# Performance work log

Hardware: AMD Instinct MI355X
Metric: run time of the kernel (lower is better)

The kernel has to match this reference:

```python
import jax, jax.numpy as jnp
import numpy as np

B, S, E, H = 4, 2048, 1024, 16
D = E // H  # head dim = 64
STRIDE, EXPR = 128, 32


def build_sparse_mask(S, stride=STRIDE, expr=EXPR):
    """Fairseq SparseMultiheadAttention fixed pattern, is_bidirectional=False.
    True = attention allowed (mask value 0), False = -inf."""
    def ckpt(i):
        if i % stride == 0 and i != 0:
            return i - expr
        return (i // stride) * stride + stride - expr

    def summaries(amax):
        s = set()
        c = ckpt(0)
        while c <= amax - 1:
            s.update(range(c, min(c + expr + 1, amax)))
            c = ckpt(c + stride)
        return s

    m = np.zeros((S, S), dtype=bool)
    for i in range(S):
        amax = i + 1  # causal (not bidirectional)
        r = ((i + stride) // stride) * stride
        if i % stride == 0 and i != 0:
            one = set(range(i - stride, min(amax, i + 1)))
        else:
            one = set(range(max(0, r - stride), min(amax, r + 1)))
        idx = sorted(one | summaries(amax))
        m[i, idx] = True
    return m


def setup_inputs() -> dict:
    key = jax.random.key(0)
    ks = jax.random.split(key, 12)
    sc = 0.02
    inp = {
        "x": jax.random.normal(ks[0], (B, S, E), dtype=jnp.float32),
        "ln1_g": jnp.ones((E,), jnp.float32), "ln1_b": jnp.zeros((E,), jnp.float32),
        "ln2_g": jnp.ones((E,), jnp.float32), "ln2_b": jnp.zeros((E,), jnp.float32),
        "wq": jax.random.normal(ks[1], (E, E), jnp.float32) * sc, "bq": jnp.zeros((E,), jnp.float32),
        "wk": jax.random.normal(ks[2], (E, E), jnp.float32) * sc, "bk": jnp.zeros((E,), jnp.float32),
        "wv": jax.random.normal(ks[3], (E, E), jnp.float32) * sc, "bv": jnp.zeros((E,), jnp.float32),
        "wo": jax.random.normal(ks[4], (E, E), jnp.float32) * sc, "bo": jnp.zeros((E,), jnp.float32),
        "w_fc": jax.random.normal(ks[5], (4 * E, E), jnp.float32) * sc, "b_fc": jnp.zeros((4 * E,), jnp.float32),
        "w_proj": jax.random.normal(ks[6], (E, 4 * E), jnp.float32) * sc, "b_proj": jnp.zeros((E,), jnp.float32),
        "mask": jnp.asarray(build_sparse_mask(S)),
    }
    return inp


def _ln(x, g, b, eps=1e-5):
    mu = jnp.mean(x, axis=-1, keepdims=True)
    var = jnp.var(x, axis=-1, keepdims=True)
    return (x - mu) * jax.lax.rsqrt(var + eps) * g + b


def _new_gelu(x):
    c = np.sqrt(2.0 / np.pi).astype(np.float32)
    return 0.5 * x * (1.0 + jnp.tanh(c * (x + 0.044715 * x ** 3)))


def reference(x, ln1_g, ln1_b, ln2_g, ln2_b, wq, bq, wk, bk, wv, bv, wo, bo,
              w_fc, b_fc, w_proj, b_proj, mask):
    # x: [B,S,E]. Note: Block residual uses ln_1(x), not raw x (x is reassigned).
    h = _ln(x, ln1_g, ln1_b)
    scale = D ** -0.5
    q = ((h @ wq.T + bq) * scale).reshape(B, S, H, D)
    k = (h @ wk.T + bk).reshape(B, S, H, D)
    v = (h @ wv.T + bv).reshape(B, S, H, D)
    scores = jnp.einsum("bqhd,bkhd->bhqk", q, k)
    scores = jnp.where(mask[None, None], scores, -jnp.inf)  # fixed sparse pattern
    p = jax.nn.softmax(scores, axis=-1)
    attn = jnp.einsum("bhqk,bkhd->bqhd", p, v).reshape(B, S, E)
    attn = attn @ wo.T + bo
    h = h + attn
    # MLP (dropout in eval mode = identity)
    y = _new_gelu(_ln(h, ln2_g, ln2_b) @ w_fc.T + b_fc) @ w_proj.T + b_proj
    return h + y
```

## Files before the change

kernel.cpp:

```cpp
#include <hip/hip_runtime.h>
#include <hip/hip_bf16.h>

#define B_ 4
#define S_ 2048
#define E_ 1024
#define H_ 16
#define D_ 64

typedef __bf16 bf16x8 __attribute__((ext_vector_type(8)));
typedef __bf16 bf16x4 __attribute__((ext_vector_type(4)));
typedef float  f32x4  __attribute__((ext_vector_type(4)));

__device__ __forceinline__ void gl_lds16(const void* g, void* l) {
  __builtin_amdgcn_global_load_lds((const __attribute__((address_space(1))) void*)g,
                                   (__attribute__((address_space(3))) void*)l, 16, 0, 0);
}

__global__ __launch_bounds__(256) void ln_kernel(const float* __restrict__ x,
                                                 const float* __restrict__ g,
                                                 const float* __restrict__ b,
                                                 float* __restrict__ o,
                                                 __bf16* __restrict__ ohi,
                                                 __bf16* __restrict__ olo) {
  int row = blockIdx.x;
  int t = threadIdx.x;
  const float* xr = x + (size_t)row * E_;
  float4 v = *(const float4*)(xr + t * 4);
  float s  = v.x + v.y + v.z + v.w;
  float ss = v.x * v.x + v.y * v.y + v.z * v.z + v.w * v.w;
#pragma unroll
  for (int off = 1; off < 64; off <<= 1) {
    s  += __shfl_xor(s, off);
    ss += __shfl_xor(ss, off);
  }
  __shared__ float sh[8];
  if ((t & 63) == 0) { sh[t >> 6] = s; sh[4 + (t >> 6)] = ss; }
  __syncthreads();
  s  = sh[0] + sh[1] + sh[2] + sh[3];
  ss = sh[4] + sh[5] + sh[6] + sh[7];
  float mu  = s * (1.0f / E_);
  float var = ss * (1.0f / E_) - mu * mu;
  float rstd = rsqrtf(var + 1e-5f);
  float4 gg = *(const float4*)(g + t * 4);
  float4 bb = *(const float4*)(b + t * 4);
  float ov[4];
  ov[0] = (v.x - mu) * rstd * gg.x + bb.x;
  ov[1] = (v.y - mu) * rstd * gg.y + bb.y;
  ov[2] = (v.z - mu) * rstd * gg.z + bb.z;
  ov[3] = (v.w - mu) * rstd * gg.w + bb.w;
  size_t base = (size_t)row * E_ + t * 4;
  if (o) *(float4*)(o + base) = make_float4(ov[0], ov[1], ov[2], ov[3]);
  if (ohi) {
    bf16x4 hv, lv;
#pragma unroll
    for (int j = 0; j < 4; ++j) {
      __bf16 hh = (__bf16)ov[j];
      hv[j] = hh;
      lv[j] = (__bf16)(ov[j] - (float)hh);
    }
    *(bf16x4*)(ohi + base) = hv;
    *(bf16x4*)(olo + base) = lv;
  }
}

__global__ __launch_bounds__(256) void split_kernel(const float* __restrict__ in,
                                                    __bf16* __restrict__ hi,
                                                    __bf16* __restrict__ lo,
                                                    int n4) {
  int idx = blockIdx.x * 256 + threadIdx.x;
  int stride = gridDim.x * 256;
  for (int i = idx; i < n4; i += stride) {
    float4 v = ((const float4*)in)[i];
    bf16x4 hv, lv;
#pragma unroll
    for (int j = 0; j < 4; ++j) {
      float f = (&v.x)[j];
      __bf16 hh = (__bf16)f;
      hv[j] = hh;
      lv[j] = (__bf16)(f - (float)hh);
    }
    ((bf16x4*)hi)[i] = hv;
    ((bf16x4*)lo)[i] = lv;
  }
}

template <int BM>
__global__ __launch_bounds__(512, 2) void gemm3(
    const __bf16* __restrict__ Ah, const __bf16* __restrict__ Al,
    const __bf16* __restrict__ Bh, const __bf16* __restrict__ Bl,
    int N, int K,
    const float* __restrict__ b0, const float* __restrict__ b1,
    const float* __restrict__ b2,
    const float* __restrict__ res, float* __restrict__ Cf,
    __bf16* __restrict__ C0h, __bf16* __restrict__ C0l,
    __bf16* __restrict__ C1h, __bf16* __restrict__ C1l,
    __bf16* __restrict__ C2h, __bf16* __restrict__ C2l,
    int act, int qkv) {
  constexpr int MI    = BM / 32;
  constexpr int MPP   = MI / 4;
  constexpr int AR    = BM / 64;
  constexpr int RND   = AR + 4;
  constexpr int AU    = BM * 8;
  constexpr int BUFU  = AU + 2048;
  constexpr int MTLOG = (BM == 256) ? 5 : 6;
  constexpr int LOGBM = (BM == 256) ? 8 : 7;

  __shared__ bf16x8 lds[2 * BUFU];

  const int t = threadIdx.x;
  const int l = t & 63;
  const int w = t >> 6;
  const int wr = w >> 2, wc = w & 3;
  const int fr = l & 15, kq = l >> 4;

  const int nwg = gridDim.x;
  const int cpx = nwg >> 3;
  const int bid = blockIdx.x;
  const int swz = (bid & 7) * cpx + (bid >> 3);
  const int mt  = swz & ((1 << MTLOG) - 1);
  const int ntl = swz >> MTLOG;
  const int row0 = mt * BM, col0 = ntl * 256;

  const int ktp = K >> 6;
  const int nt3 = 3 * ktp;

  f32x4 acc[MI][4];
#pragma unroll
  for (int i = 0; i < MI; ++i)
#pragma unroll
    for (int j = 0; j < 4; ++j) acc[i][j] = (f32x4){0.f, 0.f, 0.f, 0.f};

  auto STAGE = [&](const __bf16* Ax, const __bf16* Bx, int k0, int q, int buf) {
    if (q < AR) {
      int u = q * 512 + t;
      int row = u & (BM - 1), kg = u >> LOGBM;
      gl_lds16(Ax + (size_t)(row0 + row) * K + k0 + kg * 8,
               &lds[buf * BUFU + q * 512 + (t & 448)]);
    } else {
      int qb = q - AR;
      int u = qb * 512 + t;
      int col = u & 255, kg = u >> 8;
      gl_lds16(Bx + (size_t)(col0 + col) * K + k0 + kg * 8,
               &lds[buf * BUFU + AU + qb * 512 + (t & 448)]);
    }
  };

#pragma unroll
  for (int q = 0; q < RND; ++q) STAGE(Ah, Bh, 0, q, 0);

  int cur = 0;
  int k0n = 64, pn = 0;
  if (ktp == 1) { k0n = 0; pn = 1; }

  for (int kt = 0; kt < nt3; ++kt) {
    const bool notlast = (kt + 1 < nt3);
    const __bf16* An = (pn == 2) ? Al : Ah;
    const __bf16* Bn = (pn == 1) ? Bl : Bh;
    const int nxt = cur ^ 1;
    bf16x8 bfr[4][2];
#pragma unroll
    for (int p = 0; p < 4; ++p) {
      if (notlast) {
        if (2 * p < RND)     STAGE(An, Bn, k0n, 2 * p, nxt);
        if (2 * p + 1 < RND) STAGE(An, Bn, k0n, 2 * p + 1, nxt);
      }
      if (p == 0) {
        if (notlast) asm volatile("s_waitcnt vmcnt(2)" ::: "memory");
        else         asm volatile("s_waitcnt vmcnt(0)" ::: "memory");
        __builtin_amdgcn_s_barrier();
        asm volatile("" ::: "memory");
#pragma unroll
        for (int ni = 0; ni < 4; ++ni)
#pragma unroll
          for (int ks = 0; ks < 2; ++ks)
            bfr[ni][ks] = lds[cur * BUFU + AU + (ks * 4 + kq) * 256 + wc * 64 + ni * 16 + fr];
      }
      bf16x8 af[MPP][2];
#pragma unroll
      for (int mm = 0; mm < MPP; ++mm)
#pragma unroll
        for (int ks = 0; ks < 2; ++ks)
          af[mm][ks] = lds[cur * BUFU + (ks * 4 + kq) * BM + wr * (BM / 2) + (p * MPP + mm) * 16 + fr];
      __builtin_amdgcn_s_setprio(1);
#pragma unroll
      for (int mm = 0; mm < MPP; ++mm)
#pragma unroll
        for (int ni = 0; ni < 4; ++ni)
#pragma unroll
          for (int ks = 0; ks < 2; ++ks)
            acc[p * MPP + mm][ni] = __builtin_amdgcn_mfma_f32_16x16x32_bf16(
                af[mm][ks], bfr[ni][ks], acc[p * MPP + mm][ni], 0, 0, 0);
      __builtin_amdgcn_s_setprio(0);
    }
    asm volatile("" ::: "memory");
    __builtin_amdgcn_s_barrier();
    asm volatile("" ::: "memory");
    cur = nxt;
    k0n += 64;
    if (k0n == K) { k0n = 0; ++pn; }
  }

#pragma unroll
  for (int mi = 0; mi < MI; ++mi) {
    const int rowb = row0 + wr * (BM / 2) + mi * 16 + kq * 4;
#pragma unroll
    for (int ni = 0; ni < 4; ++ni) {
      const int col = col0 + wc * 64 + ni * 16 + fr;
#pragma unroll
      for (int r = 0; r < 4; ++r) {
        const int grow = rowb + r;
        float v = acc[mi][ni][r];
        if (qkv) {
          const int seg = col >> 10, ci = col & 1023;
          float bias = (seg == 0) ? b0[ci] : (seg == 1) ? b1[ci] : b2[ci];
          v += bias;
          if (seg == 0) v *= 0.125f;
          __bf16 hh = (__bf16)v;
          __bf16 ll = (__bf16)(v - (float)hh);
          size_t off = (size_t)grow * 1024 + ci;
          if (seg == 0)      { C0h[off] = hh; C0l[off] = ll; }
          else if (seg == 1) { C1h[off] = hh; C1l[off] = ll; }
          else {
            int bb2 = grow >> 11, ii = grow & 2047;
            int h2i = ci >> 6, dd = ci & 63;
            size_t offt = ((((size_t)bb2 * H_ + h2i) * D_ + dd) << 11) + ii;
            C2h[offt] = hh; C2l[offt] = ll;
          }
        } else {
          v += b0[col];
          if (act) {
            float zn = 0.7978845608028654f * (v + 0.044715f * v * v * v);
            float e = __expf(fminf(2.f * zn, 80.f));
            v = v * e / (e + 1.f);
          }
          size_t off = (size_t)grow * N + col;
          if (res) v += res[off];
          if (Cf) Cf[off] = v;
          if (C0h) {
            __bf16 hh = (__bf16)v;
            C0h[off] = hh;
            C0l[off] = (__bf16)(v - (float)hh);
          }
        }
      }
    }
  }
}

__device__ __forceinline__ bool sp_allowed(int i, int j) {
  if (j > i) return false;
  bool local;
  if ((i & 127) == 0 && i != 0) local = (j >= i - 128);
  else                          local = (j >= ((i >> 7) << 7));
  int jm = j & 127;
  bool summ = (j >= 96) && ((jm >= 96) || (jm == 0 && j >= 128));
  return local || summ;
}

__global__ __launch_bounds__(256) void attn_mfma(
    const __bf16* __restrict__ qhi, const __bf16* __restrict__ qlo,
    const __bf16* __restrict__ khi, const __bf16* __restrict__ klo,
    const __bf16* __restrict__ vth, const __bf16* __restrict__ vtl,
    __bf16* __restrict__ abhi, __bf16* __restrict__ ablo) {
  const int qt = blockIdx.x;
  const int h  = blockIdx.y;
  const int b  = blockIdx.z;
  const int t = threadIdx.x;
  const int l = t & 63;
  const int w = t >> 6;
  const int lanelo = l & 15, lanehi = l >> 4;

  __shared__ bf16x8 KhL[512], KlL[512], VhL[512], VlL[512];
  __shared__ __align__(16) __bf16 Pl[4][16][72];

  const int arow = qt * 64 + w * 16 + lanelo;
  size_t qoff = ((size_t)(b * S_ + arow)) * E_ + h * D_ + lanehi * 8;
  bf16x8 qh[2], ql[2];
  qh[0] = *(const bf16x8*)(qhi + qoff);      qh[1] = *(const bf16x8*)(qhi + qoff + 32);
  ql[0] = *(const bf16x8*)(qlo + qoff);      ql[1] = *(const bf16x8*)(qlo + qoff + 32);

  const int drow = qt * 64 + w * 16 + lanehi * 4;

  f32x4 o_acc[4];
#pragma unroll
  for (int n = 0; n < 4; ++n) o_acc[n] = (f32x4){0.f, 0.f, 0.f, 0.f};
  float mrow[4] = {-1e30f, -1e30f, -1e30f, -1e30f};
  float lrow[4] = {0.f, 0.f, 0.f, 0.f};

  const int nnear0 = (qt >= 2) ? (qt - 2) : 0;
  const int L = (qt - 2) * 64;
  int tmax = 0, nfar = 0;
  if (L > 96) {
    tmax = (L - 96 + 127) >> 7;
    nfar = (5 * tmax + 7) >> 3;
  }
  const int ntiles = nfar + (qt - nnear0 + 1);

  for (int tile = 0; tile < ntiles; ++tile) {
    const bool is_far = tile < nfar;
    const int jb = nnear0 + (tile - nfar);

    if (w < 2) {
      int c = l, jg; bool valid;
      if (is_far) {
        unsigned g8 = tile * 8 + (c >> 3);
        unsigned t5 = g8 / 5u, u = g8 - t5 * 5u;
        int oo = (int)(u * 8) + (c & 7);
        jg = 96 + ((int)t5 << 7) + oo;
        valid = (g8 < 5u * (unsigned)tmax) && (oo <= 32) && (jg < L);
      } else { jg = (jb << 6) + c; valid = true; }
      int tok = b * S_ + (valid ? jg : 0);
      const __bf16* src = (w == 0 ? khi : klo) + (size_t)tok * E_ + h * D_;
      bf16x8* dst = (w == 0 ? KhL : KlL);
#pragma unroll
      for (int dg = 0; dg < 8; ++dg) gl_lds16(src + dg * 8, dst + dg * 64);
    } else {
      const __bf16* src = (w == 2 ? vth : vtl) + ((size_t)((b * H_ + h) * D_ + l)) * S_;
      bf16x8* dst = (w == 2 ? VhL : VlL);
#pragma unroll
      for (int jgp = 0; jgp < 8; ++jgp) {
        int j0;
        if (is_far) {
          unsigned g8 = tile * 8 + jgp;
          unsigned t5 = g8 / 5u, u = g8 - t5 * 5u;
          j0 = (g8 < 5u * (unsigned)tmax) ? (96 + ((int)t5 << 7) + (int)u * 8) : 0;
        } else j0 = (jb << 6) + jgp * 8;
        gl_lds16(src + j0, dst + jgp * 64);
      }
    }
    __syncthreads();

    f32x4 s[4];
#pragma unroll
    for (int n = 0; n < 4; ++n) s[n] = (f32x4){0.f, 0.f, 0.f, 0.f};
#pragma unroll
    for (int ks = 0; ks < 2; ++ks) {
#pragma unroll
      for (int n = 0; n < 4; ++n) {
        bf16x8 kb_h = KhL[(4 * ks + lanehi) * 64 + n * 16 + lanelo];
        bf16x8 kb_l = KlL[(4 * ks + lanehi) * 64 + n * 16 + lanelo];
        s[n] = __builtin_amdgcn_mfma_f32_16x16x32_bf16(qh[ks], kb_h, s[n], 0, 0, 0);
        s[n] = __builtin_amdgcn_mfma_f32_16x16x32_bf16(qh[ks], kb_l, s[n], 0, 0, 0);
        s[n] = __builtin_amdgcn_mfma_f32_16x16x32_bf16(ql[ks], kb_h, s[n], 0, 0, 0);
      }
    }

    int jgc[4]; bool vldc[4], summc[4];
#pragma unroll
    for (int n = 0; n < 4; ++n) {
      int c = n * 16 + lanelo;
      if (is_far) {
        unsigned g8 = tile * 8 + (c >> 3);
        unsigned t5 = g8 / 5u, u = g8 - t5 * 5u;
        int oo = (int)(u * 8) + (c & 7);
        int jg = 96 + ((int)t5 << 7) + oo;
        jgc[n] = jg;
        vldc[n] = (g8 < 5u * (unsigned)tmax) && (oo <= 32) && (jg < L);
        summc[n] = true;
      } else {
        int jg = (jb << 6) + c;
        jgc[n] = jg; vldc[n] = true;
        int jm = jg & 127;
        summc[n] = (jg >= 96) && ((jm >= 96) || (jm == 0 && jg >= 128));
      }
    }
    float tm[4] = {-1e30f, -1e30f, -1e30f, -1e30f};
#pragma unroll
    for (int r = 0; r < 4; ++r) {
      int i = drow + r;
      int lb = (((i & 127) == 0) && i != 0) ? (i - 128) : ((i >> 7) << 7);
#pragma unroll
      for (int n = 0; n < 4; ++n) {
        bool ok = is_far ? vldc[n]
                         : ((jgc[n] <= i) && ((jgc[n] >= lb) || summc[n]));
        float sv = ok ? s[n][r] : -1e30f;
        s[n][r] = sv;
        tm[r] = fmaxf(tm[r], sv);
      }
    }
#pragma unroll
    for (int off = 1; off < 16; off <<= 1)
#pragma unroll
      for (int r = 0; r < 4; ++r) tm[r] = fmaxf(tm[r], __shfl_xor(tm[r], off));

    float psum[4] = {0.f, 0.f, 0.f, 0.f};
#pragma unroll
    for (int r = 0; r < 4; ++r) {
      float mnew = fmaxf(mrow[r], tm[r]);
      float alpha = __expf(mrow[r] - mnew);
      mrow[r] = mnew;
      lrow[r] *= alpha;
#pragma unroll
      for (int n = 0; n < 4; ++n) o_acc[n][r] *= alpha;
#pragma unroll
      for (int n = 0; n < 4; ++n) {
        float sv = s[n][r];
        float p = (sv > -1e29f) ? __expf(sv - mnew) : 0.f;
        s[n][r] = p;
        psum[r] += p;
      }
    }
#pragma unroll
    for (int off = 1; off < 16; off <<= 1)
#pragma unroll
      for (int r = 0; r < 4; ++r) psum[r] += __shfl_xor(psum[r], off);
#pragma unroll
    for (int r = 0; r < 4; ++r) lrow[r] += psum[r];

#pragma unroll
    for (int r = 0; r < 4; ++r)
#pragma unroll
      for (int n = 0; n < 4; ++n)
        Pl[w][lanehi * 4 + r][n * 16 + lanelo] = (__bf16)s[n][r];
    bf16x8 pa[2];
    pa[0] = *(const bf16x8*)&Pl[w][lanelo][8 * lanehi];
    pa[1] = *(const bf16x8*)&Pl[w][lanelo][8 * lanehi + 32];

#pragma unroll
    for (int ks = 0; ks < 2; ++ks) {
#pragma unroll
      for (int n = 0; n < 4; ++n) {
        bf16x8 vb_h = VhL[(4 * ks + lanehi) * 64 + n * 16 + lanelo];
        bf16x8 vb_l = VlL[(4 * ks + lanehi) * 64 + n * 16 + lanelo];
        o_acc[n] = __builtin_amdgcn_mfma_f32_16x16x32_bf16(pa[ks], vb_h, o_acc[n], 0, 0, 0);
        o_acc[n] = __builtin_amdgcn_mfma_f32_16x16x32_bf16(pa[ks], vb_l, o_acc[n], 0, 0, 0);
      }
    }
    __syncthreads();
  }

#pragma unroll
  for (int r = 0; r < 4; ++r) {
    float inv = 1.0f / lrow[r];
    int i = drow + r;
    size_t rb = ((size_t)(b * S_ + i)) * E_ + h * D_;
#pragma unroll
    for (int n = 0; n < 4; ++n) {
      float val = o_acc[n][r] * inv;
      __bf16 hh = (__bf16)val;
      abhi[rb + n * 16 + lanelo] = hh;
      ablo[rb + n * 16 + lanelo] = (__bf16)(val - (float)hh);
    }
  }
}

extern "C" void kernel_launch(void* const* d_in, const int* in_sizes, int n_in,
                              void* d_out, int out_size, void* d_ws, size_t ws_size,
                              hipStream_t stream) {
  const float* x      = (const float*)d_in[0];
  const float* ln1_g  = (const float*)d_in[1];
  const float* ln1_b  = (const float*)d_in[2];
  const float* ln2_g  = (const float*)d_in[3];
  const float* ln2_b  = (const float*)d_in[4];
  const float* wq     = (const float*)d_in[5];
  const float* bq     = (const float*)d_in[6];
  const float* wk     = (const float*)d_in[7];
  const float* bk     = (const float*)d_in[8];
  const float* wv     = (const float*)d_in[9];
  const float* bv     = (const float*)d_in[10];
  const float* wo     = (const float*)d_in[11];
  const float* bo     = (const float*)d_in[12];
  const float* w_fc   = (const float*)d_in[13];
  const float* b_fc   = (const float*)d_in[14];
  const float* w_proj = (const float*)d_in[15];
  const float* b_proj = (const float*)d_in[16];

  char* W = (char*)d_ws;
  const size_t MB = (size_t)1 << 20;
  const int NTOK = B_ * S_;

  float*  h      = (float*)(W + 0 * MB);
  __bf16* h_hi   = (__bf16*)(W + 32 * MB);
  __bf16* h_lo   = (__bf16*)(W + 48 * MB);
  __bf16* q_hi   = (__bf16*)(W + 64 * MB);
  __bf16* q_lo   = (__bf16*)(W + 80 * MB);
  __bf16* k_hi   = (__bf16*)(W + 96 * MB);
  __bf16* k_lo   = (__bf16*)(W + 112 * MB);
  __bf16* vt_hi  = (__bf16*)(W + 128 * MB);
  __bf16* vt_lo  = (__bf16*)(W + 144 * MB);
  __bf16* ab_hi  = h_hi;
  __bf16* ab_lo  = h_lo;
  float*  h2     = (float*)(W + 64 * MB);
  __bf16* l2o_hi = (__bf16*)(W + 0 * MB);
  __bf16* l2o_lo = (__bf16*)(W + 16 * MB);
  __bf16* fcb_hi = (__bf16*)(W + 96 * MB);
  __bf16* fcb_lo = (__bf16*)(W + 160 * MB);
  __bf16* wqkv_hi = (__bf16*)(W + 160 * MB);
  __bf16* wqkv_lo = (__bf16*)(W + 166 * MB);
  __bf16* wo_hi  = (__bf16*)(W + 172 * MB);
  __bf16* wo_lo  = (__bf16*)(W + 174 * MB);
  __bf16* wfc_hi = (__bf16*)(W + 32 * MB);
  __bf16* wfc_lo = (__bf16*)(W + 40 * MB);
  __bf16* wpj_hi = (__bf16*)(W + 32 * MB);
  __bf16* wpj_lo = (__bf16*)(W + 40 * MB);
  float* out = (float*)d_out;

  const int SPLIT_BLKS = 2048;
  const int nw1 = E_ * E_ / 4;
  const int nw4 = 4 * E_ * E_ / 4;
  const int WSEG = E_ * E_;

  ln_kernel<<<NTOK, 256, 0, stream>>>(x, ln1_g, ln1_b, h, h_hi, h_lo);

  split_kernel<<<SPLIT_BLKS, 256, 0, stream>>>(wq, wqkv_hi, wqkv_lo, nw1);
  split_kernel<<<SPLIT_BLKS, 256, 0, stream>>>(wk, wqkv_hi + WSEG, wqkv_lo + WSEG, nw1);
  split_kernel<<<SPLIT_BLKS, 256, 0, stream>>>(wv, wqkv_hi + 2 * WSEG, wqkv_lo + 2 * WSEG, nw1);
  gemm3<256><<<384, 512, 0, stream>>>(h_hi, h_lo, wqkv_hi, wqkv_lo, 3072, E_,
                                      bq, bk, bv, nullptr, nullptr,
                                      q_hi, q_lo, k_hi, k_lo, vt_hi, vt_lo, 0, 1);

  attn_mfma<<<dim3(S_ / 64, H_, B_), 256, 0, stream>>>(q_hi, q_lo, k_hi, k_lo,
                                                       vt_hi, vt_lo, ab_hi, ab_lo);

  split_kernel<<<SPLIT_BLKS, 256, 0, stream>>>(wo, wo_hi, wo_lo, nw1);
  gemm3<128><<<256, 512, 0, stream>>>(ab_hi, ab_lo, wo_hi, wo_lo, E_, E_,
                                      bo, nullptr, nullptr, h, h2,
                                      nullptr, nullptr, nullptr, nullptr, nullptr, nullptr, 0, 0);

  ln_kernel<<<NTOK, 256, 0, stream>>>(h2, ln2_g, ln2_b, nullptr, l2o_hi, l2o_lo);

  split_kernel<<<SPLIT_BLKS, 256, 0, stream>>>(w_fc, wfc_hi, wfc_lo, nw4);
  gemm3<256><<<512, 512, 0, stream>>>(l2o_hi, l2o_lo, wfc_hi, wfc_lo, 4 * E_, E_,
                                      b_fc, nullptr, nullptr, nullptr, nullptr,
                                      fcb_hi, fcb_lo, nullptr, nullptr, nullptr, nullptr, 1, 0);

  split_kernel<<<SPLIT_BLKS, 256, 0, stream>>>(w_proj, wpj_hi, wpj_lo, nw4);
  gemm3<128><<<256, 512, 0, stream>>>(fcb_hi, fcb_lo, wpj_hi, wpj_lo, E_, 4 * E_,
                                      b_proj, nullptr, nullptr, h2, out,
                                      nullptr, nullptr, nullptr, nullptr, nullptr, nullptr, 0, 0);
}
```

Measured before the change: 1.469 ms.

## Restructure GEMM k-loop into four barrier-separated phases interleaving staging and MFMA

Splits each 64-wide k-tile in the hi/lo split-bf16 GEMM into four phases, one per k-half and m-half pair. Each phase loads its own A fragments and, where needed, B fragments from LDS. Global-to-LDS staging for the next tile is issued after each phase's LDS reads, and a barrier separates phases. The aim is to smooth memory/compute interleaving and reduce register pressure from double-held fragments, at the cost of more barriers per tile.

After: 1.496 ms. About the same (+1.8%).

```diff
diff --git a/kernel.cpp b/kernel.cpp
--- a/kernel.cpp
+++ b/kernel.cpp
@@ -85,7 +85,7 @@
 }
 
 template <int BM>
-__global__ __launch_bounds__(512, 2) void gemm3(
+__global__ __launch_bounds__(512, 2) void gemm8(
     const __bf16* __restrict__ Ah, const __bf16* __restrict__ Al,
     const __bf16* __restrict__ Bh, const __bf16* __restrict__ Bl,
     int N, int K,
@@ -97,7 +97,7 @@
     __bf16* __restrict__ C2h, __bf16* __restrict__ C2l,
     int act, int qkv) {
   constexpr int MI    = BM / 32;
-  constexpr int MPP   = MI / 4;
+  constexpr int MH    = MI / 2;
   constexpr int AR    = BM / 64;
   constexpr int RND   = AR + 4;
   constexpr int AU    = BM * 8;
@@ -157,44 +157,51 @@
     const __bf16* An = (pn == 2) ? Al : Ah;
     const __bf16* Bn = (pn == 1) ? Bl : Bh;
     const int nxt = cur ^ 1;
-    bf16x8 bfr[4][2];
+    bf16x8 bfr[4];
 #pragma unroll
     for (int p = 0; p < 4; ++p) {
-      if (notlast) {
-        if (2 * p < RND)     STAGE(An, Bn, k0n, 2 * p, nxt);
-        if (2 * p + 1 < RND) STAGE(An, Bn, k0n, 2 * p + 1, nxt);
-      }
+      const int ks = p >> 1, mh = p & 1;
+      bf16x8 af[MH];
       if (p == 0) {
-        if (notlast) asm volatile("s_waitcnt vmcnt(2)" ::: "memory");
-        else         asm volatile("s_waitcnt vmcnt(0)" ::: "memory");
+        if (notlast) {
+          STAGE(An, Bn, k0n, 0, nxt);
+          STAGE(An, Bn, k0n, 1, nxt);
+          asm volatile("s_waitcnt vmcnt(2)" ::: "memory");
+        } else {
+          asm volatile("s_waitcnt vmcnt(0)" ::: "memory");
+        }
         __builtin_amdgcn_s_barrier();
-        asm volatile("" ::: "memory");
 #pragma unroll
         for (int ni = 0; ni < 4; ++ni)
-#pragma unroll
-          for (int ks = 0; ks < 2; ++ks)
-            bfr[ni][ks] = lds[cur * BUFU + AU + (ks * 4 + kq) * 256 + wc * 64 + ni * 16 + fr];
-      }
-      bf16x8 af[MPP][2];
-#pragma unroll
-      for (int mm = 0; mm < MPP; ++mm)
-#pragma unroll
-        for (int ks = 0; ks < 2; ++ks)
-          af[mm][ks] = lds[cur * BUFU + (ks * 4 + kq) * BM + wr * (BM / 2) + (p * MPP + mm) * 16 + fr];
+          bfr[ni] = lds[cur * BUFU + AU + (ks * 4 + kq) * 256 + wc * 64 + ni * 16 + fr];
+#pragma unroll
+        for (int mm = 0; mm < MH; ++mm)
+          af[mm] = lds[cur * BUFU + (ks * 4 + kq) * BM + wr * (BM / 2) + (mh * MH + mm) * 16 + fr];
+      } else {
+        if (mh == 0) {
+#pragma unroll
+          for (int ni = 0; ni < 4; ++ni)
+            bfr[ni] = lds[cur * BUFU + AU + (ks * 4 + kq) * 256 + wc * 64 + ni * 16 + fr];
+        }
+#pragma unroll
+        for (int mm = 0; mm < MH; ++mm)
+          af[mm] = lds[cur * BUFU + (ks * 4 + kq) * BM + wr * (BM / 2) + (mh * MH + mm) * 16 + fr];
+        if (notlast) {
+          if (2 * p < RND)     STAGE(An, Bn, k0n, 2 * p, nxt);
+          if (2 * p + 1 < RND) STAGE(An, Bn, k0n, 2 * p + 1, nxt);
+        }
+        __builtin_amdgcn_s_barrier();
+      }
       __builtin_amdgcn_s_setprio(1);
 #pragma unroll
-      for (int mm = 0; mm < MPP; ++mm)
+      for (int mm = 0; mm < MH; ++mm)
 #pragma unroll
         for (int ni = 0; ni < 4; ++ni)
-#pragma unroll
-          for (int ks = 0; ks < 2; ++ks)
-            acc[p * MPP + mm][ni] = __builtin_amdgcn_mfma_f32_16x16x32_bf16(
-                af[mm][ks], bfr[ni][ks], acc[p * MPP + mm][ni], 0, 0, 0);
+          acc[mh * MH + mm][ni] = __builtin_amdgcn_mfma_f32_16x16x32_bf16(
+              af[mm], bfr[ni], acc[mh * MH + mm][ni], 0, 0, 0);
       __builtin_amdgcn_s_setprio(0);
-    }
-    asm volatile("" ::: "memory");
-    __builtin_amdgcn_s_barrier();
-    asm volatile("" ::: "memory");
+      __builtin_amdgcn_s_barrier();
+    }
     cur = nxt;
     k0n += 64;
     if (k0n == K) { k0n = 0; ++pn; }
@@ -505,7 +512,7 @@
   split_kernel<<<SPLIT_BLKS, 256, 0, stream>>>(wq, wqkv_hi, wqkv_lo, nw1);
   split_kernel<<<SPLIT_BLKS, 256, 0, stream>>>(wk, wqkv_hi + WSEG, wqkv_lo + WSEG, nw1);
   split_kernel<<<SPLIT_BLKS, 256, 0, stream>>>(wv, wqkv_hi + 2 * WSEG, wqkv_lo + 2 * WSEG, nw1);
-  gemm3<256><<<384, 512, 0, stream>>>(h_hi, h_lo, wqkv_hi, wqkv_lo, 3072, E_,
+  gemm8<256><<<384, 512, 0, stream>>>(h_hi, h_lo, wqkv_hi, wqkv_lo, 3072, E_,
                                       bq, bk, bv, nullptr, nullptr,
                                       q_hi, q_lo, k_hi, k_lo, vt_hi, vt_lo, 0, 1);
 
@@ -513,19 +520,19 @@
                                                        vt_hi, vt_lo, ab_hi, ab_lo);
 
   split_kernel<<<SPLIT_BLKS, 256, 0, stream>>>(wo, wo_hi, wo_lo, nw1);
-  gemm3<128><<<256, 512, 0, stream>>>(ab_hi, ab_lo, wo_hi, wo_lo, E_, E_,
+  gemm8<128><<<256, 512, 0, stream>>>(ab_hi, ab_lo, wo_hi, wo_lo, E_, E_,
                                       bo, nullptr, nullptr, h, h2,
                                       nullptr, nullptr, nullptr, nullptr, nullptr, nullptr, 0, 0);
 
   ln_kernel<<<NTOK, 256, 0, stream>>>(h2, ln2_g, ln2_b, nullptr, l2o_hi, l2o_lo);
 
   split_kernel<<<SPLIT_BLKS, 256, 0, stream>>>(w_fc, wfc_hi, wfc_lo, nw4);
-  gemm3<256><<<512, 512, 0, stream>>>(l2o_hi, l2o_lo, wfc_hi, wfc_lo, 4 * E_, E_,
+  gemm8<256><<<512, 512, 0, stream>>>(l2o_hi, l2o_lo, wfc_hi, wfc_lo, 4 * E_, E_,
                                       b_fc, nullptr, nullptr, nullptr, nullptr,
                                       fcb_hi, fcb_lo, nullptr, nullptr, nullptr, nullptr, 1, 0);
 
   split_kernel<<<SPLIT_BLKS, 256, 0, stream>>>(w_proj, wpj_hi, wpj_lo, nw4);
-  gemm3<128><<<256, 512, 0, stream>>>(fcb_hi, fcb_lo, wpj_hi, wpj_lo, E_, 4 * E_,
+  gemm8<128><<<256, 512, 0, stream>>>(fcb_hi, fcb_lo, wpj_hi, wpj_lo, E_, 4 * E_,
                                       b_proj, nullptr, nullptr, h2, out,
                                       nullptr, nullptr, nullptr, nullptr, nullptr, nullptr, 0, 0);
 }
```
